# Kernel optimization log

Hardware: AMD Instinct MI355X
Metric: run time of the kernel (lower is better)

## Reference

```python
import jax, jax.numpy as jnp
import numpy as np

B, T, D, H = 2, 2048, 1024, 16
HD = D // H
DFF = 4 * D
EPS = 1e-5


def gelu_tanh(x):
    c = jnp.sqrt(2.0 / jnp.pi).astype(x.dtype)
    return 0.5 * x * (1.0 + jnp.tanh(c * (x + 0.044715 * x ** 3)))


def layernorm(x, scale, shift):
    mean = jnp.mean(x, axis=-1, keepdims=True)
    var = jnp.var(x, axis=-1, keepdims=True)  # unbiased=False
    return (x - mean) / jnp.sqrt(var + EPS) * scale + shift


def setup_inputs() -> dict:
    key = jax.random.key(0)
    ks = jax.random.split(key, 12)
    s = lambda fan_in: 1.0 / np.sqrt(fan_in)
    return {
        "x": jax.random.normal(ks[0], (B, T, D), jnp.float32),
        "wq": jax.random.normal(ks[1], (D, D), jnp.float32) * s(D),
        "wk": jax.random.normal(ks[2], (D, D), jnp.float32) * s(D),
        "wv": jax.random.normal(ks[3], (D, D), jnp.float32) * s(D),
        "wo": jax.random.normal(ks[4], (D, D), jnp.float32) * s(D),
        "bo": jnp.zeros((D,), jnp.float32),
        "ln1_scale": jnp.ones((D,), jnp.float32),
        "ln1_shift": jnp.zeros((D,), jnp.float32),
        "ln2_scale": jnp.ones((D,), jnp.float32),
        "ln2_shift": jnp.zeros((D,), jnp.float32),
        "w1": jax.random.normal(ks[5], (D, DFF), jnp.float32) * s(D),
        "b1": jnp.zeros((DFF,), jnp.float32),
        "w2": jax.random.normal(ks[6], (DFF, D), jnp.float32) * s(DFF),
        "b2": jnp.zeros((D,), jnp.float32),
    }


def reference(x, wq, wk, wv, wo, bo, ln1_scale, ln1_shift, ln2_scale, ln2_shift, w1, b1, w2, b2):
    # pre-LN attention
    h = layernorm(x, ln1_scale, ln1_shift)
    q = (h @ wq).reshape(B, T, H, HD).transpose(0, 2, 1, 3)  # [B,H,T,hd]
    k = (h @ wk).reshape(B, T, H, HD).transpose(0, 2, 1, 3)
    v = (h @ wv).reshape(B, T, H, HD).transpose(0, 2, 1, 3)
    scores = jnp.einsum('bhqd,bhkd->bhqk', q, k) / jnp.sqrt(jnp.float32(HD))
    causal = jnp.tril(jnp.ones((T, T), bool))
    scores = jnp.where(causal, scores, -jnp.inf)
    attn = jax.nn.softmax(scores, axis=-1)
    ctx = jnp.einsum('bhqk,bhkd->bhqd', attn, v)
    ctx = ctx.transpose(0, 2, 1, 3).reshape(B, T, D)
    attn_out = ctx @ wo + bo
    x = x + attn_out  # dropout p=0
    # pre-LN FFN
    h2 = layernorm(x, ln2_scale, ln2_shift)
    ff = gelu_tanh(h2 @ w1 + b1) @ w2 + b2
    return x + ff
```

## Files before the change

kernel.cpp:

```cpp
#include <hip/hip_runtime.h>
#include <hip/hip_bf16.h>
#include <stdint.h>

typedef unsigned short u16;
typedef __attribute__((ext_vector_type(8))) short s16x8;
typedef __attribute__((ext_vector_type(4))) float f32x4;

#define B_   2
#define T_   2048
#define D_   1024
#define H_   16
#define HD_  64
#define DFF_ 4096
#define M_   (B_*T_)

#define SC2F 0.18033688f

__device__ __forceinline__ u16 f2b(float f){
  uint32_t u = __float_as_uint(f);
  u += 0x7FFFu + ((u >> 16) & 1u);
  return (u16)(u >> 16);
}
__device__ __forceinline__ float b2f(u16 u){ return __uint_as_float(((uint32_t)u) << 16); }
__device__ __forceinline__ uint32_t pk2(float lo, float hi){
  uint32_t r;
  asm volatile("v_cvt_pk_bf16_f32 %0, %1, %2" : "=v"(r) : "v"(lo), "v"(hi));
  return r;
}

__device__ __forceinline__ void gl_lds16(const void* g, void* l){
  __builtin_amdgcn_global_load_lds((const __attribute__((address_space(1))) void*)g,
                                   (__attribute__((address_space(3))) void*)l, 16, 0, 0);
}

template<int N> __device__ __forceinline__ void waitvm(){
  if constexpr (N == 0)      asm volatile("s_waitcnt vmcnt(0)" ::: "memory");
  else if constexpr (N == 2) asm volatile("s_waitcnt vmcnt(2)" ::: "memory");
  else if constexpr (N == 4) asm volatile("s_waitcnt vmcnt(4)" ::: "memory");
  else                       asm volatile("s_waitcnt vmcnt(8)" ::: "memory");
}

__device__ __forceinline__ void wconv_tile(const float* __restrict__ W, u16* __restrict__ Wt,
                                           int K, int N, int tk, int tn, int tid,
                                           u16* __restrict__ tile ){
  const int k0 = tk << 6, n0 = tn << 6;
  const int rr = tid >> 4, c4 = (tid & 15) << 2;
  #pragma unroll
  for (int rep = 0; rep < 4; rep++){
    int r = rr + (rep << 4);
    float4 v = *reinterpret_cast<const float4*>(W + (size_t)(k0 + r)*N + n0 + c4);
    tile[r*68 + c4+0] = f2b(v.x); tile[r*68 + c4+1] = f2b(v.y);
    tile[r*68 + c4+2] = f2b(v.z); tile[r*68 + c4+3] = f2b(v.w);
  }
  __syncthreads();
  const int rn = tid >> 2, kb = (tid & 3) << 4;
  u16 tmp[16];
  #pragma unroll
  for (int j = 0; j < 16; j++) tmp[j] = tile[(kb + j)*68 + rn];
  ushort4* dst = reinterpret_cast<ushort4*>(Wt + (size_t)(n0 + rn)*K + k0 + kb);
  dst[0] = make_ushort4(tmp[0], tmp[1], tmp[2], tmp[3]);
  dst[1] = make_ushort4(tmp[4], tmp[5], tmp[6], tmp[7]);
  dst[2] = make_ushort4(tmp[8], tmp[9], tmp[10], tmp[11]);
  dst[3] = make_ushort4(tmp[12], tmp[13], tmp[14], tmp[15]);
}

__global__ __launch_bounds__(256) void wconv_all(const float* __restrict__ wq,
                                                 const float* __restrict__ wk,
                                                 const float* __restrict__ wv,
                                                 const float* __restrict__ wo,
                                                 u16* __restrict__ wqkvT, u16* __restrict__ woT,
                                                 const float* __restrict__ x,
                                                 const float* __restrict__ ln1s,
                                                 const float* __restrict__ ln1b,
                                                 u16* __restrict__ hout){
  const int bid = blockIdx.x;
  const int tid = threadIdx.x;
  if (bid >= 1024){
    const int row = bid - 1024;
    float4 a = reinterpret_cast<const float4*>(x + ((size_t)row << 10))[tid];
    float s = a.x + a.y + a.z + a.w;
    float q = a.x*a.x + a.y*a.y + a.z*a.z + a.w*a.w;
    #pragma unroll
    for (int o = 32; o > 0; o >>= 1){ s += __shfl_xor(s, o); q += __shfl_xor(q, o); }
    __shared__ float red[8];
    const int w = tid >> 6;
    if ((tid & 63) == 0){ red[w] = s; red[4 + w] = q; }
    __syncthreads();
    float S = red[0] + red[1] + red[2] + red[3];
    float Q = red[4] + red[5] + red[6] + red[7];
    float mean = S * (1.0f/1024.0f);
    float var  = Q * (1.0f/1024.0f) - mean*mean;
    float inv = rsqrtf(var + 1e-5f);
    float4 gsc = reinterpret_cast<const float4*>(ln1s)[tid];
    float4 gsh = reinterpret_cast<const float4*>(ln1b)[tid];
    ushort4 o4;
    o4.x = f2b((a.x - mean)*inv*gsc.x + gsh.x);
    o4.y = f2b((a.y - mean)*inv*gsc.y + gsh.y);
    o4.z = f2b((a.z - mean)*inv*gsc.z + gsh.z);
    o4.w = f2b((a.w - mean)*inv*gsc.w + gsh.w);
    reinterpret_cast<ushort4*>(hout + ((size_t)row << 10))[tid] = o4;
    return;
  }
  __shared__ u16 tile[64*68];
  const int which = bid >> 8, t = bid & 255;
  const float* W = (which == 0) ? wq : (which == 1) ? wk : (which == 2) ? wv : wo;
  u16* Wt = (which == 3) ? woT : wqkvT + (size_t)which * D_ * D_;
  wconv_tile(W, Wt, 1024, 1024, t >> 4, t & 15, tid, tile);
}

__global__ __launch_bounds__(256) void reduce2(const u16* __restrict__ p,
                                               const float* __restrict__ bias,
                                               const u16* __restrict__ resid,
                                               float* __restrict__ out){
  const size_t idx = ((size_t)blockIdx.x << 8) + threadIdx.x;
  ushort4 a4 = reinterpret_cast<const ushort4*>(p)[idx];
  ushort4 b4 = reinterpret_cast<const ushort4*>(p)[idx + (((size_t)M_*D_) >> 2)];
  ushort4 r4 = reinterpret_cast<const ushort4*>(resid)[idx];
  float4 bb = reinterpret_cast<const float4*>(bias)[threadIdx.x];
  float4 o;
  o.x = b2f(a4.x) + b2f(b4.x) + b2f(r4.x) + bb.x;
  o.y = b2f(a4.y) + b2f(b4.y) + b2f(r4.y) + bb.y;
  o.z = b2f(a4.z) + b2f(b4.z) + b2f(r4.z) + bb.z;
  o.w = b2f(a4.w) + b2f(b4.w) + b2f(r4.w) + bb.w;
  reinterpret_cast<float4*>(out)[idx] = o;
}

__global__ __launch_bounds__(256) void reduce_ln(const u16* __restrict__ p,
                                                 const float* __restrict__ bias,
                                                 const float* __restrict__ resid,
                                                 const float* __restrict__ sc,
                                                 const float* __restrict__ sh,
                                                 u16* __restrict__ x1,
                                                 u16* __restrict__ h2){
  const int row = blockIdx.x;
  const int tid = threadIdx.x;
  const size_t idx = ((size_t)row << 8) + tid;
  ushort4 a4 = reinterpret_cast<const ushort4*>(p)[idx];
  ushort4 b4 = reinterpret_cast<const ushort4*>(p)[idx + (((size_t)M_*D_) >> 2)];
  float4 r  = reinterpret_cast<const float4*>(resid)[idx];
  float4 bb = reinterpret_cast<const float4*>(bias)[tid];
  float4 v;
  v.x = b2f(a4.x) + b2f(b4.x) + r.x + bb.x;
  v.y = b2f(a4.y) + b2f(b4.y) + r.y + bb.y;
  v.z = b2f(a4.z) + b2f(b4.z) + r.z + bb.z;
  v.w = b2f(a4.w) + b2f(b4.w) + r.w + bb.w;
  ushort4 xo;
  xo.x = f2b(v.x); xo.y = f2b(v.y); xo.z = f2b(v.z); xo.w = f2b(v.w);
  reinterpret_cast<ushort4*>(x1)[idx] = xo;
  float s = v.x + v.y + v.z + v.w;
  float q = v.x*v.x + v.y*v.y + v.z*v.z + v.w*v.w;
  #pragma unroll
  for (int o = 32; o > 0; o >>= 1){ s += __shfl_xor(s, o); q += __shfl_xor(q, o); }
  __shared__ float red[8];
  const int w = tid >> 6;
  if ((tid & 63) == 0){ red[w] = s; red[4 + w] = q; }
  __syncthreads();
  float S = red[0] + red[1] + red[2] + red[3];
  float Q = red[4] + red[5] + red[6] + red[7];
  float mean = S * (1.0f/1024.0f);
  float var  = Q * (1.0f/1024.0f) - mean*mean;
  float inv = rsqrtf(var + 1e-5f);
  float4 gsc = reinterpret_cast<const float4*>(sc)[tid];
  float4 gsh = reinterpret_cast<const float4*>(sh)[tid];
  ushort4 o4;
  o4.x = f2b((v.x - mean)*inv*gsc.x + gsh.x);
  o4.y = f2b((v.y - mean)*inv*gsc.y + gsh.y);
  o4.z = f2b((v.z - mean)*inv*gsc.z + gsh.z);
  o4.w = f2b((v.w - mean)*inv*gsc.w + gsh.w);
  reinterpret_cast<ushort4*>(h2 + ((size_t)row << 10))[tid] = o4;
}

template<int EPI, int NF>
__global__ __launch_bounds__(512, 2) void gemm8(const u16* __restrict__ A, const u16* __restrict__ Bt,
                                                const float* __restrict__ bias,
                                                void* __restrict__ Cv, void* __restrict__ Cv2,
                                                const float* __restrict__ cw1,
                                                const float* __restrict__ cw2,
                                                u16* __restrict__ w1T, u16* __restrict__ w2T,
                                                int M, int N, int K, int lda){
  constexpr int BROWS = NF * 32;
  __shared__ __align__(16) u16 LA[2][2][128*64];
  __shared__ __align__(16) u16 LB[2][2][BROWS*64];
  const int tid = threadIdx.x;

  if constexpr (EPI == 1){
    if (blockIdx.x >= 192){
      const int tid256 = tid & 255, sel2 = tid >> 8;
      u16* tile = &LA[0][0][0] + sel2 * (64*68);
      const int t = ((int)blockIdx.x - 192)*2 + sel2;
      if (t < 1024) wconv_tile(cw1, w1T, 1024, 4096, t >> 6, t & 63, tid256, tile);
      else          wconv_tile(cw2, w2T, 4096, 1024, (t-1024) >> 4, (t-1024) & 15, tid256, tile);
      return;
    }
  }

  const int lane = tid & 63;
  const int w = tid >> 6;
  const int wm = w >> 2, wn = w & 3;
  const int g = lane >> 4, l15 = lane & 15;
  const int bnb = (wn & 1) * (NF * 16);

  int tn, tm, kz;
  if constexpr (EPI == 1){
    const int flat = blockIdx.x;
    const int nfid = (flat & 7) * 24 + (flat >> 3);
    tn = nfid % 12; tm = nfid / 12; kz = 0;
  } else {
    const int nx = gridDim.x, ny = gridDim.y;
    const int nwg = nx * ny * gridDim.z;
    const int flat = blockIdx.x + nx * (blockIdx.y + ny * blockIdx.z);
    const int nfid = (flat & 7) * (nwg >> 3) + (flat >> 3);
    tn = nfid % nx;
    const int rest = nfid / nx;
    tm = rest % ny;
    kz = rest / ny;
  }
  const int tn0 = tn * (NF * 64);
  const int tm0 = tm << 8;
  const u16* Az = A  + (size_t)kz * K;
  const u16* Bz = Bt + (size_t)kz * K;

  const int arow0 = tid >> 3,         asl0 = (((tid) & 7) ^ (arow0 & 7)) << 3;
  const int arow1 = (tid + 512) >> 3, asl1 = (((tid + 512) & 7) ^ (arow1 & 7)) << 3;

  f32x4 acc[8][NF];
  #pragma unroll
  for (int i = 0; i < 8; i++)
    #pragma unroll
    for (int j = 0; j < NF; j++) acc[i][j] = (f32x4){0.f,0.f,0.f,0.f};
  s16x8 bf[NF][2];
  constexpr int WVN = (NF == 4) ? 8 : 2;

#define STG_A(db, h, tt) do{                                                        \
    gl_lds16(Az + (size_t)(tm0 + (h)*128 + arow0)*lda + ((tt) << 6) + asl0,         \
             &LA[db][h][tid*8]);                                                    \
    gl_lds16(Az + (size_t)(tm0 + (h)*128 + arow1)*lda + ((tt) << 6) + asl1,         \
             &LA[db][h][(tid + 512)*8]);                                            \
  }while(0)
#define STG_B(db, h, tt) do{                                                        \
    gl_lds16(Bz + (size_t)(tn0 + (h)*BROWS + arow0)*lda + ((tt) << 6) + asl0,       \
             &LB[db][h][tid*8]);                                                    \
    if constexpr (NF == 4){                                                         \
      gl_lds16(Bz + (size_t)(tn0 + (h)*BROWS + arow1)*lda + ((tt) << 6) + asl1,     \
               &LB[db][h][(tid + 512)*8]);                                          \
    }                                                                               \
  }while(0)
#define LDAF(db, mf, kk) (*reinterpret_cast<const s16x8*>(                          \
    &LA[db][wm][((mf)*16 + l15)*64 + ((((kk)*4 + g) ^ (l15 & 7)) << 3)]))
#define LDBF(db, nf, kk) (*reinterpret_cast<const s16x8*>(                          \
    &LB[db][wn >> 1][(bnb + (nf)*16 + l15)*64 + ((((kk)*4 + g) ^ (l15 & 7)) << 3)]))
#define BLOAD(db) do{ _Pragma("unroll")                                             \
    for (int nf = 0; nf < NF; nf++){ bf[nf][0] = LDBF(db, nf, 0);                   \
                                     bf[nf][1] = LDBF(db, nf, 1); } }while(0)
#define PH(db, MFA, MFB, STG, WV) do{                                               \
    s16x8 a00 = LDAF(db, MFA, 0), a01 = LDAF(db, MFA, 1);                           \
    s16x8 a10 = LDAF(db, MFB, 0), a11 = LDAF(db, MFB, 1);                           \
    STG;                                                                            \
    WV;                                                                             \
    __builtin_amdgcn_s_barrier();                                                   \
    __builtin_amdgcn_s_setprio(1);                                                  \
    _Pragma("unroll")                                                               \
    for (int nf = 0; nf < NF; nf++){                                                \
      acc[MFA][nf] = __builtin_amdgcn_mfma_f32_16x16x32_bf16(a00, bf[nf][0], acc[MFA][nf], 0,0,0); \
      acc[MFA][nf] = __builtin_amdgcn_mfma_f32_16x16x32_bf16(a01, bf[nf][1], acc[MFA][nf], 0,0,0); \
      acc[MFB][nf] = __builtin_amdgcn_mfma_f32_16x16x32_bf16(a10, bf[nf][0], acc[MFB][nf], 0,0,0); \
      acc[MFB][nf] = __builtin_amdgcn_mfma_f32_16x16x32_bf16(a11, bf[nf][1], acc[MFB][nf], 0,0,0); \
    }                                                                               \
    __builtin_amdgcn_s_setprio(0);                                                  \
    __builtin_amdgcn_s_barrier();                                                   \
  }while(0)

  const int NT = K >> 6;
  STG_B(0, 0, 0); STG_B(0, 1, 0); STG_A(0, 0, 0); STG_A(0, 1, 0);
  STG_B(1, 0, 1); STG_B(1, 1, 1);
  waitvm<NF>();
  __builtin_amdgcn_s_barrier();

  for (int t = 0; t < NT; t += 2){
    const bool last = (t + 2 >= NT);
    BLOAD(0);
    PH(0, 0, 1, STG_A(1, 0, t + 1), );
    PH(0, 2, 3, STG_A(1, 1, t + 1), );
    PH(0, 4, 5, if (!last) STG_B(0, 0, t + 2), );
    PH(0, 6, 7, if (!last) STG_B(0, 1, t + 2),
                if (last) waitvm<0>(); else waitvm<WVN>(););
    BLOAD(1);
    PH(1, 0, 1, if (!last) STG_A(0, 0, t + 2), );
    PH(1, 2, 3, if (!last) STG_A(0, 1, t + 2), );
    PH(1, 4, 5, if (!last) STG_B(1, 0, t + 3), );
    PH(1, 6, 7, if (!last) STG_B(1, 1, t + 3),
                if (last) waitvm<0>(); else waitvm<WVN>(););
  }
#undef STG_A
#undef STG_B
#undef LDAF
#undef LDBF
#undef BLOAD
#undef PH

  if constexpr (EPI == 1){
    const int sel = tn0 >> 10;
    if (sel < 2){
      #pragma unroll
      for (int mf = 0; mf < 8; mf++){
        const int mb = tm0 + wm*128 + mf*16 + (g << 2);
        #pragma unroll
        for (int nf = 0; nf < NF; nf++){
          const int n = tn0 + wn*(NF*16) + nf*16 + l15;
          const int nn = n & 1023;
          const int hh = nn >> 6, d = nn & 63;
          #pragma unroll
          for (int rr = 0; rr < 4; rr++){
            const int m = mb + rr;
            float v = acc[mf][nf][rr];
            if (sel == 0) v *= SC2F;
            ((u16*)Cv)[(size_t)sel*((size_t)M_*D_) +
                       ((((size_t)(m >> 11)*H_ + hh)*T_ + (m & 2047)) << 6) + d] = f2b(v);
          }
        }
      }
    } else {
      u16* TR = &LA[0][0][0];
      u16* vt = (u16*)Cv2;
      const int bq = tm0 >> 11;
      const int tloc = tm0 & 2047;
      #pragma unroll
      for (int hp = 0; hp < 2; hp++){
        __syncthreads();
        if ((wn >> 1) == hp){
          #pragma unroll
          for (int mf = 0; mf < 8; mf++){
            const int mb = wm*128 + mf*16 + (g << 2);
            #pragma unroll
            for (int nf = 0; nf < NF; nf++){
              const int nr = ((wn & 1) << 6) + (nf << 4) + l15;
              #pragma unroll
              for (int rr = 0; rr < 4; rr++){
                const int m = mb + rr;
                TR[nr*256 + (((m >> 3) ^ (nr & 15)) << 3) + (m & 7)] = f2b(acc[mf][nf][rr]);
              }
            }
          }
        }
        __syncthreads();
        {
          const int nr = tid >> 2;
          const int m0 = (tid & 3) << 6;
          const int nn = (tn0 & 1023) + (hp << 7) + nr;
          const int hh = nn >> 6, d = nn & 63;
          u16* dst = vt + (((size_t)(bq*H_ + hh))*HD_ + d)*T_ + tloc + m0;
          #pragma unroll
          for (int jj = 0; jj < 8; jj++){
            const int j = (m0 >> 3) + jj;
            s16x8 vv = *reinterpret_cast<const s16x8*>(&TR[nr*256 + ((j ^ (nr & 15)) << 3)]);
            *reinterpret_cast<s16x8*>(dst + jj*8) = vv;
          }
        }
      }
    }
  } else {
    #pragma unroll
    for (int mf = 0; mf < 8; mf++){
      const int mb = tm0 + wm*128 + mf*16 + (g << 2);
      #pragma unroll
      for (int nf = 0; nf < NF; nf++){
        const int n = tn0 + wn*(NF*16) + nf*16 + l15;
        #pragma unroll
        for (int rr = 0; rr < 4; rr++){
          const int m = mb + rr;
          float v = acc[mf][nf][rr];
          if constexpr (EPI == 0){
            ((u16*)Cv)[(size_t)kz*((size_t)M*N) + (size_t)m*N + n] = f2b(v);
          } else {
            float u = v + bias[n];
            float t2 = 0.7978845608f*(u + 0.044715f*u*u*u);
            float e = __expf(2.0f*t2);
            float th = 1.0f - 2.0f/(e + 1.0f);
            ((u16*)Cv)[(size_t)m*N + n] = f2b(0.5f*u*(1.0f + th));
          }
        }
      }
    }
  }
}

__global__ __launch_bounds__(512) void attn_k(const u16* __restrict__ Qg, const u16* __restrict__ Kg,
                                              const u16* __restrict__ Vg, u16* __restrict__ ctx){
  const int flat = blockIdx.x + (blockIdx.y << 3);
  const int xcd = flat & 7, j_ = (flat >> 3) & 3, pr_ = flat >> 5;
  const int bh  = (j_ << 3) + xcd;
  const int tid = threadIdx.x;
  const int lane = tid & 63;
  const int w = tid >> 6;
  const int g = lane >> 4, l15 = lane & 15;

  __shared__ __align__(16) u16 Qs[128*64];
  __shared__ __align__(16) u16 Ks[2][128*64];
  __shared__ __align__(16) u16 Vt[2][64*128];
  __shared__ __align__(16) u16 Pl[8][16*128];
  u16* const Plw = &Pl[w][0];

  const size_t hb = (size_t)bh * ((size_t)T_*HD_);
  const u16* Qh = Qg + hb;
  const u16* Kh = Kg + hb;
  const u16* Vh = Vg + hb;
  const int b = bh >> 4, hh = bh & 15;

  const int qk_r0 = tid >> 3,         qk_c0 = (((tid) & 7) ^ (qk_r0 & 7)) << 3;
  const int qk_r1 = (tid + 512) >> 3, qk_c1 = (((tid + 512) & 7) ^ (qk_r1 & 7)) << 3;
  const int v_r0 = tid >> 4,          v_c0 = (((tid) & 15) ^ (v_r0 & 7)) << 3;
  const int v_r1 = (tid + 512) >> 4,  v_c1 = (((tid + 512) & 15) ^ (v_r1 & 7)) << 3;

  for (int ph = 0; ph < 2; ++ph){
    const int qt = ph ? (15 - pr_) : pr_;
    const int NKT = qt + 1;

    gl_lds16(Qh + (size_t)(qt*128 + qk_r0)*HD_ + qk_c0, Qs + tid*8);
    gl_lds16(Qh + (size_t)(qt*128 + qk_r1)*HD_ + qk_c1, Qs + (tid+512)*8);
    gl_lds16(Kh + (size_t)qk_r0*HD_ + qk_c0, Ks[0] + tid*8);
    gl_lds16(Kh + (size_t)qk_r1*HD_ + qk_c1, Ks[0] + (tid+512)*8);
    gl_lds16(Vh + (size_t)v_r0*T_ + v_c0, Vt[0] + tid*8);
    gl_lds16(Vh + (size_t)v_r1*T_ + v_c1, Vt[0] + (tid+512)*8);
    __syncthreads();

    s16x8 qa[2];
    #pragma unroll
    for (int kk = 0; kk < 2; kk++){
      int ra = (w << 4) + l15;
      int slot = (kk << 2) + g;
      qa[kk] = *reinterpret_cast<const s16x8*>(Qs + ra*64 + ((slot ^ (ra & 7)) << 3));
    }

    f32x4 accO[4];
    #pragma unroll
    for (int j = 0; j < 4; j++) accO[j] = (f32x4){0.f,0.f,0.f,0.f};
    float mrow = -1e30f, lrow = 0.f;
    const int qgl = qt*128 + (w << 4) + l15;

    for (int kt = 0; kt < NKT; ++kt){
      const int cur = kt & 1, nxt = cur ^ 1;
      const bool pf = (kt + 1 < NKT);

      if (pf){
        gl_lds16(Kh + (size_t)((kt+1)*128 + qk_r0)*HD_ + qk_c0, Ks[nxt] + tid*8);
        gl_lds16(Kh + (size_t)((kt+1)*128 + qk_r1)*HD_ + qk_c1, Ks[nxt] + (tid+512)*8);
        gl_lds16(Vh + (size_t)v_r0*T_ + (kt+1)*128 + v_c0, Vt[nxt] + tid*8);
        gl_lds16(Vh + (size_t)v_r1*T_ + (kt+1)*128 + v_c1, Vt[nxt] + (tid+512)*8);
      }

      f32x4 accS[8];
      #pragma unroll
      for (int j = 0; j < 8; j++) accS[j] = (f32x4){0.f,0.f,0.f,0.f};
      __builtin_amdgcn_s_setprio(1);
      #pragma unroll
      for (int jn = 0; jn < 8; jn++){
        #pragma unroll
        for (int kk = 0; kk < 2; kk++){
          int rb = (jn << 4) + l15;
          int slot = (kk << 2) + g;
          s16x8 kf = *reinterpret_cast<const s16x8*>(Ks[cur] + rb*64 + ((slot ^ (rb & 7)) << 3));
          accS[jn] = __builtin_amdgcn_mfma_f32_16x16x32_bf16(kf, qa[kk], accS[jn], 0, 0, 0);
        }
      }
      __builtin_amdgcn_s_setprio(0);

      if (kt == qt){
        #pragma unroll
        for (int jn = 0; jn < 8; jn++)
          #pragma unroll
          for (int rr = 0; rr < 4; rr++){
            int kgl = kt*128 + (jn << 4) + (g << 2) + rr;
            if (kgl > qgl) accS[jn][rr] = -1e30f;
          }
      }

      float rmax = accS[0][0];
      #pragma unroll
      for (int jn = 0; jn < 8; jn++)
        #pragma unroll
        for (int rr = 0; rr < 4; rr++) rmax = fmaxf(rmax, accS[jn][rr]);
      rmax = fmaxf(rmax, __shfl_xor(rmax, 16));
      rmax = fmaxf(rmax, __shfl_xor(rmax, 32));

      if (__any(rmax > mrow + 8.0f)){
        float mn = fmaxf(mrow, rmax);
        float sf = exp2f(mrow - mn);
        mrow = mn;
        lrow *= sf;
        #pragma unroll
        for (int rr = 0; rr < 4; rr++){
          float sfr = __shfl(sf, ((lane >> 4) << 2) + rr);
          #pragma unroll
          for (int jn = 0; jn < 4; jn++) accO[jn][rr] *= sfr;
        }
      }

      float tsum = 0.f;
      #pragma unroll
      for (int jn = 0; jn < 8; jn++){
        float pv0 = exp2f(accS[jn][0] - mrow);
        float pv1 = exp2f(accS[jn][1] - mrow);
        float pv2 = exp2f(accS[jn][2] - mrow);
        float pv3 = exp2f(accS[jn][3] - mrow);
        tsum += (pv0 + pv1) + (pv2 + pv3);
        int ch = ((jn << 1) | (g >> 1)) ^ (l15 & 7);
        int base = (l15 << 7) + (ch << 3) + ((g & 1) << 2);
        uint2 pkd = make_uint2(pk2(pv0, pv1), pk2(pv2, pv3));
        *reinterpret_cast<uint2*>(&Plw[base]) = pkd;
      }
      tsum += __shfl_xor(tsum, 16);
      tsum += __shfl_xor(tsum, 32);
      lrow += tsum;

      __builtin_amdgcn_s_setprio(1);
      #pragma unroll
      for (int kk = 0; kk < 4; kk++){
        int pch = ((kk << 2) + g) ^ (l15 & 7);
        s16x8 pa = *reinterpret_cast<const s16x8*>(&Plw[(l15 << 7) + (pch << 3)]);
        #pragma unroll
        for (int jn = 0; jn < 4; jn++){
          int vd = (jn << 4) + l15;
          int vslot = (((kk << 2) + g) & 8) | ((((kk << 2) + g) ^ (vd & 7)) & 7);
          s16x8 vbf = *reinterpret_cast<const s16x8*>(Vt[cur] + (vd << 7) + (vslot << 3));
          accO[jn] = __builtin_amdgcn_mfma_f32_16x16x32_bf16(pa, vbf, accO[jn], 0, 0, 0);
        }
      }
      __builtin_amdgcn_s_setprio(0);

      __syncthreads();
    }

    #pragma unroll
    for (int rr = 0; rr < 4; rr++){
      float lr = __shfl(lrow, ((lane >> 4) << 2) + rr);
      float inv = 1.0f / lr;
      int qrow = qt*128 + (w << 4) + (g << 2) + rr;
      size_t rowbase = ((size_t)(b*T_ + qrow) << 10) + ((size_t)hh << 6);
      #pragma unroll
      for (int jn = 0; jn < 4; jn++){
        int d = (jn << 4) + l15;
        ctx[rowbase + d] = f2b(accO[jn][rr] * inv);
      }
    }
  }
}

extern "C" void kernel_launch(void* const* d_in, const int* in_sizes, int n_in,
                              void* d_out, int out_size, void* d_ws, size_t ws_size,
                              hipStream_t stream){
  (void)in_sizes; (void)n_in; (void)out_size; (void)ws_size;
  const float* x    = (const float*)d_in[0];
  const float* wq   = (const float*)d_in[1];
  const float* wk   = (const float*)d_in[2];
  const float* wv   = (const float*)d_in[3];
  const float* wo   = (const float*)d_in[4];
  const float* bo   = (const float*)d_in[5];
  const float* ln1s = (const float*)d_in[6];
  const float* ln1b = (const float*)d_in[7];
  const float* ln2s = (const float*)d_in[8];
  const float* ln2b = (const float*)d_in[9];
  const float* w1   = (const float*)d_in[10];
  const float* b1   = (const float*)d_in[11];
  const float* w2   = (const float*)d_in[12];
  const float* b2   = (const float*)d_in[13];
  float* out = (float*)d_out;

  char* p = (char*)d_ws;
  u16*  wqkvT = (u16*)p;  p += (size_t)3*D_*D_*2;
  u16*  woT   = (u16*)p;  p += (size_t)D_*D_*2;
  u16*  w1T   = (u16*)p;  p += (size_t)D_*DFF_*2;
  u16*  w2T   = (u16*)p;  p += (size_t)DFF_*D_*2;
  u16*  h     = (u16*)p;  p += (size_t)M_*D_*2;
  u16*  qb    = (u16*)p;  p += (size_t)M_*D_*2;
  u16*  kb    = (u16*)p;  p += (size_t)M_*D_*2;
  u16*  vb    = (u16*)p;  p += (size_t)M_*D_*2;
  u16*  ctx   = (u16*)p;  p += (size_t)M_*D_*2;
  u16*  x1    = (u16*)p;  p += (size_t)M_*D_*2;
  u16*  h2    = (u16*)p;  p += (size_t)M_*D_*2;
  u16*  ff1   = (u16*)p;  p += (size_t)M_*DFF_*2;
  (void)kb; (void)vb;
  u16* part = h;

  dim3 blk(256), blk8(512);
  wconv_all<<<1024 + M_, blk, 0, stream>>>(wq, wk, wv, wo, wqkvT, woT, x, ln1s, ln1b, h);
  gemm8<1,4><<<192 + 1024, blk8, 0, stream>>>(h, wqkvT, nullptr, qb, ff1,
                                              w1, w2, w1T, w2T, M_, 3*D_, D_, D_);
  attn_k<<<dim3(8,32), blk8, 0, stream>>>(qb, qb + (size_t)M_*D_, ff1, ctx);
  gemm8<0,2><<<dim3(8,16,2), blk8, 0, stream>>>(ctx, woT, nullptr, part, nullptr,
                                                nullptr, nullptr, nullptr, nullptr,
                                                M_, D_, D_/2, D_);
  reduce_ln<<<M_, blk, 0, stream>>>(part, bo, x, ln2s, ln2b, x1, h2);
  gemm8<3,4><<<dim3(16,16,1), blk8, 0, stream>>>(h2, w1T, b1, ff1, nullptr,
                                                 nullptr, nullptr, nullptr, nullptr,
                                                 M_, DFF_, D_, D_);
  gemm8<0,2><<<dim3(8,16,2), blk8, 0, stream>>>(ff1, w2T, nullptr, part, nullptr,
                                                nullptr, nullptr, nullptr, nullptr,
                                                M_, D_, DFF_/2, DFF_);
  reduce2<<<M_, blk, 0, stream>>>(part, b2, x1, out);
}
```

Measured before the change: 212.7 us.

## Triple-buffer K/V in attention and merge GEMM phases into fewer barriers

```diff
diff --git a/kernel.cpp b/kernel.cpp
--- a/kernel.cpp
+++ b/kernel.cpp
@@ -39,6 +39,9 @@
   else if constexpr (N == 4) asm volatile("s_waitcnt vmcnt(4)" ::: "memory");
   else                       asm volatile("s_waitcnt vmcnt(8)" ::: "memory");
 }
+#define BARRL do{ asm volatile("s_waitcnt lgkmcnt(0)" ::: "memory"); \
+                  __builtin_amdgcn_s_barrier(); \
+                  asm volatile("" ::: "memory"); }while(0)
 
 __device__ __forceinline__ void wconv_tile(const float* __restrict__ W, u16* __restrict__ Wt,
                                            int K, int N, int tk, int tn, int tid,
@@ -229,7 +232,6 @@
     #pragma unroll
     for (int j = 0; j < NF; j++) acc[i][j] = (f32x4){0.f,0.f,0.f,0.f};
   s16x8 bf[NF][2];
-  constexpr int WVN = (NF == 4) ? 8 : 2;
 
 #define STG_A(db, h, tt) do{                                                        \
     gl_lds16(Az + (size_t)(tm0 + (h)*128 + arow0)*lda + ((tt) << 6) + asl0,         \
@@ -252,19 +254,25 @@
 #define BLOAD(db) do{ _Pragma("unroll")                                             \
     for (int nf = 0; nf < NF; nf++){ bf[nf][0] = LDBF(db, nf, 0);                   \
                                      bf[nf][1] = LDBF(db, nf, 1); } }while(0)
-#define PH(db, MFA, MFB, STG, WV) do{                                               \
-    s16x8 a00 = LDAF(db, MFA, 0), a01 = LDAF(db, MFA, 1);                           \
-    s16x8 a10 = LDAF(db, MFB, 0), a11 = LDAF(db, MFB, 1);                           \
+#define PH2(db, MF0, STG, WV) do{                                                   \
+    s16x8 aA0 = LDAF(db, (MF0)+0, 0), aA1 = LDAF(db, (MF0)+0, 1);                   \
+    s16x8 aB0 = LDAF(db, (MF0)+1, 0), aB1 = LDAF(db, (MF0)+1, 1);                   \
+    s16x8 aC0 = LDAF(db, (MF0)+2, 0), aC1 = LDAF(db, (MF0)+2, 1);                   \
+    s16x8 aD0 = LDAF(db, (MF0)+3, 0), aD1 = LDAF(db, (MF0)+3, 1);                   \
     STG;                                                                            \
     WV;                                                                             \
     __builtin_amdgcn_s_barrier();                                                   \
     __builtin_amdgcn_s_setprio(1);                                                  \
     _Pragma("unroll")                                                               \
     for (int nf = 0; nf < NF; nf++){                                                \
-      acc[MFA][nf] = __builtin_amdgcn_mfma_f32_16x16x32_bf16(a00, bf[nf][0], acc[MFA][nf], 0,0,0); \
-      acc[MFA][nf] = __builtin_amdgcn_mfma_f32_16x16x32_bf16(a01, bf[nf][1], acc[MFA][nf], 0,0,0); \
-      acc[MFB][nf] = __builtin_amdgcn_mfma_f32_16x16x32_bf16(a10, bf[nf][0], acc[MFB][nf], 0,0,0); \
-      acc[MFB][nf] = __builtin_amdgcn_mfma_f32_16x16x32_bf16(a11, bf[nf][1], acc[MFB][nf], 0,0,0); \
+      acc[(MF0)+0][nf] = __builtin_amdgcn_mfma_f32_16x16x32_bf16(aA0, bf[nf][0], acc[(MF0)+0][nf], 0,0,0); \
+      acc[(MF0)+0][nf] = __builtin_amdgcn_mfma_f32_16x16x32_bf16(aA1, bf[nf][1], acc[(MF0)+0][nf], 0,0,0); \
+      acc[(MF0)+1][nf] = __builtin_amdgcn_mfma_f32_16x16x32_bf16(aB0, bf[nf][0], acc[(MF0)+1][nf], 0,0,0); \
+      acc[(MF0)+1][nf] = __builtin_amdgcn_mfma_f32_16x16x32_bf16(aB1, bf[nf][1], acc[(MF0)+1][nf], 0,0,0); \
+      acc[(MF0)+2][nf] = __builtin_amdgcn_mfma_f32_16x16x32_bf16(aC0, bf[nf][0], acc[(MF0)+2][nf], 0,0,0); \
+      acc[(MF0)+2][nf] = __builtin_amdgcn_mfma_f32_16x16x32_bf16(aC1, bf[nf][1], acc[(MF0)+2][nf], 0,0,0); \
+      acc[(MF0)+3][nf] = __builtin_amdgcn_mfma_f32_16x16x32_bf16(aD0, bf[nf][0], acc[(MF0)+3][nf], 0,0,0); \
+      acc[(MF0)+3][nf] = __builtin_amdgcn_mfma_f32_16x16x32_bf16(aD1, bf[nf][1], acc[(MF0)+3][nf], 0,0,0); \
     }                                                                               \
     __builtin_amdgcn_s_setprio(0);                                                  \
     __builtin_amdgcn_s_barrier();                                                   \
@@ -279,24 +287,20 @@
   for (int t = 0; t < NT; t += 2){
     const bool last = (t + 2 >= NT);
     BLOAD(0);
-    PH(0, 0, 1, STG_A(1, 0, t + 1), );
-    PH(0, 2, 3, STG_A(1, 1, t + 1), );
-    PH(0, 4, 5, if (!last) STG_B(0, 0, t + 2), );
-    PH(0, 6, 7, if (!last) STG_B(0, 1, t + 2),
-                if (last) waitvm<0>(); else waitvm<WVN>(););
+    PH2(0, 0, { STG_A(1, 0, t + 1); STG_A(1, 1, t + 1); }, );
+    PH2(0, 4, { if (!last){ STG_B(0, 0, t + 2); STG_B(0, 1, t + 2); } },
+              if (last) waitvm<0>(); else waitvm<NF>(););
     BLOAD(1);
-    PH(1, 0, 1, if (!last) STG_A(0, 0, t + 2), );
-    PH(1, 2, 3, if (!last) STG_A(0, 1, t + 2), );
-    PH(1, 4, 5, if (!last) STG_B(1, 0, t + 3), );
-    PH(1, 6, 7, if (!last) STG_B(1, 1, t + 3),
-                if (last) waitvm<0>(); else waitvm<WVN>(););
+    PH2(1, 0, { if (!last){ STG_A(0, 0, t + 2); STG_A(0, 1, t + 2); } }, );
+    PH2(1, 4, { if (!last){ STG_B(1, 0, t + 3); STG_B(1, 1, t + 3); } },
+              if (last) waitvm<0>(); else waitvm<NF>(););
   }
 #undef STG_A
 #undef STG_B
 #undef LDAF
 #undef LDBF
 #undef BLOAD
-#undef PH
+#undef PH2
 
   if constexpr (EPI == 1){
     const int sel = tn0 >> 10;
@@ -394,10 +398,10 @@
   const int w = tid >> 6;
   const int g = lane >> 4, l15 = lane & 15;
 
-  __shared__ __align__(16) u16 Qs[128*64];
-  __shared__ __align__(16) u16 Ks[2][128*64];
-  __shared__ __align__(16) u16 Vt[2][64*128];
   __shared__ __align__(16) u16 Pl[8][16*128];
+  __shared__ __align__(16) u16 Ks[3][128*64];
+  __shared__ __align__(16) u16 Vt[3][64*128];
+  u16* const Qs  = &Pl[0][0];
   u16* const Plw = &Pl[w][0];
 
   const size_t hb = (size_t)bh * ((size_t)T_*HD_);
@@ -411,17 +415,26 @@
   const int v_r0 = tid >> 4,          v_c0 = (((tid) & 15) ^ (v_r0 & 7)) << 3;
   const int v_r1 = (tid + 512) >> 4,  v_c1 = (((tid + 512) & 15) ^ (v_r1 & 7)) << 3;
 
+#define STG_K(buf, kt) do{                                                          \
+    gl_lds16(Kh + (size_t)((kt)*128 + qk_r0)*HD_ + qk_c0, Ks[buf] + tid*8);         \
+    gl_lds16(Kh + (size_t)((kt)*128 + qk_r1)*HD_ + qk_c1, Ks[buf] + (tid+512)*8);   \
+  }while(0)
+#define STG_V(buf, kt) do{                                                          \
+    gl_lds16(Vh + (size_t)v_r0*T_ + (kt)*128 + v_c0, Vt[buf] + tid*8);              \
+    gl_lds16(Vh + (size_t)v_r1*T_ + (kt)*128 + v_c1, Vt[buf] + (tid+512)*8);        \
+  }while(0)
+
   for (int ph = 0; ph < 2; ++ph){
     const int qt = ph ? (15 - pr_) : pr_;
     const int NKT = qt + 1;
 
+    BARRL;
     gl_lds16(Qh + (size_t)(qt*128 + qk_r0)*HD_ + qk_c0, Qs + tid*8);
     gl_lds16(Qh + (size_t)(qt*128 + qk_r1)*HD_ + qk_c1, Qs + (tid+512)*8);
-    gl_lds16(Kh + (size_t)qk_r0*HD_ + qk_c0, Ks[0] + tid*8);
-    gl_lds16(Kh + (size_t)qk_r1*HD_ + qk_c1, Ks[0] + (tid+512)*8);
-    gl_lds16(Vh + (size_t)v_r0*T_ + v_c0, Vt[0] + tid*8);
-    gl_lds16(Vh + (size_t)v_r1*T_ + v_c1, Vt[0] + (tid+512)*8);
-    __syncthreads();
+    STG_K(0, 0); STG_V(0, 0);
+    if (NKT > 1){ STG_K(1, 1); STG_V(1, 1); }
+    if (NKT > 1) waitvm<4>(); else waitvm<0>();
+    BARRL;
 
     s16x8 qa[2];
     #pragma unroll
@@ -430,6 +443,7 @@
       int slot = (kk << 2) + g;
       qa[kk] = *reinterpret_cast<const s16x8*>(Qs + ra*64 + ((slot ^ (ra & 7)) << 3));
     }
+    BARRL;
 
     f32x4 accO[4];
     #pragma unroll
@@ -437,16 +451,16 @@
     float mrow = -1e30f, lrow = 0.f;
     const int qgl = qt*128 + (w << 4) + l15;
 
+    int cur = 0, n2 = 2;
     for (int kt = 0; kt < NKT; ++kt){
-      const int cur = kt & 1, nxt = cur ^ 1;
-      const bool pf = (kt + 1 < NKT);
-
-      if (pf){
-        gl_lds16(Kh + (size_t)((kt+1)*128 + qk_r0)*HD_ + qk_c0, Ks[nxt] + tid*8);
-        gl_lds16(Kh + (size_t)((kt+1)*128 + qk_r1)*HD_ + qk_c1, Ks[nxt] + (tid+512)*8);
-        gl_lds16(Vh + (size_t)v_r0*T_ + (kt+1)*128 + v_c0, Vt[nxt] + tid*8);
-        gl_lds16(Vh + (size_t)v_r1*T_ + (kt+1)*128 + v_c1, Vt[nxt] + (tid+512)*8);
-      }
+      if (kt > 0) BARRL;
+      if (kt + 2 < NKT){ STG_K(n2, kt + 2); STG_V(n2, kt + 2); }
+      if (kt + 2 < NKT)      waitvm<8>();
+      else if (kt + 1 < NKT) waitvm<4>();
+      else                   waitvm<0>();
+
+      const u16* Kc = Ks[cur];
+      const u16* Vc = Vt[cur];
 
       f32x4 accS[8];
       #pragma unroll
@@ -458,7 +472,7 @@
         for (int kk = 0; kk < 2; kk++){
           int rb = (jn << 4) + l15;
           int slot = (kk << 2) + g;
-          s16x8 kf = *reinterpret_cast<const s16x8*>(Ks[cur] + rb*64 + ((slot ^ (rb & 7)) << 3));
+          s16x8 kf = *reinterpret_cast<const s16x8*>(Kc + rb*64 + ((slot ^ (rb & 7)) << 3));
           accS[jn] = __builtin_amdgcn_mfma_f32_16x16x32_bf16(kf, qa[kk], accS[jn], 0, 0, 0);
         }
       }
@@ -521,13 +535,14 @@
         for (int jn = 0; jn < 4; jn++){
           int vd = (jn << 4) + l15;
           int vslot = (((kk << 2) + g) & 8) | ((((kk << 2) + g) ^ (vd & 7)) & 7);
-          s16x8 vbf = *reinterpret_cast<const s16x8*>(Vt[cur] + (vd << 7) + (vslot << 3));
+          s16x8 vbf = *reinterpret_cast<const s16x8*>(Vc + (vd << 7) + (vslot << 3));
           accO[jn] = __builtin_amdgcn_mfma_f32_16x16x32_bf16(pa, vbf, accO[jn], 0, 0, 0);
         }
       }
       __builtin_amdgcn_s_setprio(0);
 
-      __syncthreads();
+      cur = (cur == 2) ? 0 : cur + 1;
+      n2  = (n2  == 2) ? 0 : n2  + 1;
     }
 
     #pragma unroll
@@ -543,6 +558,8 @@
       }
     }
   }
+#undef STG_K
+#undef STG_V
 }
 
 extern "C" void kernel_launch(void* const* d_in, const int* in_sizes, int n_in,
```

Result: faster. 205.8 us (-3.2%).

## Replace fine-grained phased GEMM pipeline with whole-tile double buffering

Applied to the files above, without the earlier changes.

```diff
diff --git a/kernel.cpp b/kernel.cpp
--- a/kernel.cpp
+++ b/kernel.cpp
@@ -34,11 +34,13 @@
 }
 
 template<int N> __device__ __forceinline__ void waitvm(){
-  if constexpr (N == 0)      asm volatile("s_waitcnt vmcnt(0)" ::: "memory");
-  else if constexpr (N == 2) asm volatile("s_waitcnt vmcnt(2)" ::: "memory");
-  else if constexpr (N == 4) asm volatile("s_waitcnt vmcnt(4)" ::: "memory");
-  else                       asm volatile("s_waitcnt vmcnt(8)" ::: "memory");
-}
+  if constexpr (N == 0)       asm volatile("s_waitcnt vmcnt(0)" ::: "memory");
+  else if constexpr (N == 4)  asm volatile("s_waitcnt vmcnt(4)" ::: "memory");
+  else if constexpr (N == 6)  asm volatile("s_waitcnt vmcnt(6)" ::: "memory");
+  else                        asm volatile("s_waitcnt vmcnt(8)" ::: "memory");
+}
+#define BARR do{ asm volatile("" ::: "memory"); __builtin_amdgcn_s_barrier(); \
+                 asm volatile("" ::: "memory"); }while(0)
 
 __device__ __forceinline__ void wconv_tile(const float* __restrict__ W, u16* __restrict__ Wt,
                                            int K, int N, int tk, int tn, int tid,
@@ -171,7 +173,7 @@
 }
 
 template<int EPI, int NF>
-__global__ __launch_bounds__(512, 2) void gemm8(const u16* __restrict__ A, const u16* __restrict__ Bt,
+__global__ __launch_bounds__(512, 1) void gemm8(const u16* __restrict__ A, const u16* __restrict__ Bt,
                                                 const float* __restrict__ bias,
                                                 void* __restrict__ Cv, void* __restrict__ Cv2,
                                                 const float* __restrict__ cw1,
@@ -228,8 +230,6 @@
   for (int i = 0; i < 8; i++)
     #pragma unroll
     for (int j = 0; j < NF; j++) acc[i][j] = (f32x4){0.f,0.f,0.f,0.f};
-  s16x8 bf[NF][2];
-  constexpr int WVN = (NF == 4) ? 8 : 2;
 
 #define STG_A(db, h, tt) do{                                                        \
     gl_lds16(Az + (size_t)(tm0 + (h)*128 + arow0)*lda + ((tt) << 6) + asl0,         \
@@ -249,54 +249,53 @@
     &LA[db][wm][((mf)*16 + l15)*64 + ((((kk)*4 + g) ^ (l15 & 7)) << 3)]))
 #define LDBF(db, nf, kk) (*reinterpret_cast<const s16x8*>(                          \
     &LB[db][wn >> 1][(bnb + (nf)*16 + l15)*64 + ((((kk)*4 + g) ^ (l15 & 7)) << 3)]))
-#define BLOAD(db) do{ _Pragma("unroll")                                             \
-    for (int nf = 0; nf < NF; nf++){ bf[nf][0] = LDBF(db, nf, 0);                   \
-                                     bf[nf][1] = LDBF(db, nf, 1); } }while(0)
-#define PH(db, MFA, MFB, STG, WV) do{                                               \
-    s16x8 a00 = LDAF(db, MFA, 0), a01 = LDAF(db, MFA, 1);                           \
-    s16x8 a10 = LDAF(db, MFB, 0), a11 = LDAF(db, MFB, 1);                           \
-    STG;                                                                            \
-    WV;                                                                             \
-    __builtin_amdgcn_s_barrier();                                                   \
+#define RUN(db) do{                                                                 \
+    s16x8 bfr[NF][2], af[8][2];                                                     \
+    _Pragma("unroll")                                                               \
+    for (int nf = 0; nf < NF; nf++){ bfr[nf][0] = LDBF(db, nf, 0);                  \
+                                     bfr[nf][1] = LDBF(db, nf, 1); }                \
+    _Pragma("unroll")                                                               \
+    for (int mf = 0; mf < 8; mf++){ af[mf][0] = LDAF(db, mf, 0);                    \
+                                    af[mf][1] = LDAF(db, mf, 1); }                  \
     __builtin_amdgcn_s_setprio(1);                                                  \
     _Pragma("unroll")                                                               \
-    for (int nf = 0; nf < NF; nf++){                                                \
-      acc[MFA][nf] = __builtin_amdgcn_mfma_f32_16x16x32_bf16(a00, bf[nf][0], acc[MFA][nf], 0,0,0); \
-      acc[MFA][nf] = __builtin_amdgcn_mfma_f32_16x16x32_bf16(a01, bf[nf][1], acc[MFA][nf], 0,0,0); \
-      acc[MFB][nf] = __builtin_amdgcn_mfma_f32_16x16x32_bf16(a10, bf[nf][0], acc[MFB][nf], 0,0,0); \
-      acc[MFB][nf] = __builtin_amdgcn_mfma_f32_16x16x32_bf16(a11, bf[nf][1], acc[MFB][nf], 0,0,0); \
-    }                                                                               \
+    for (int mf = 0; mf < 8; mf++)                                                  \
+      _Pragma("unroll")                                                             \
+      for (int nf = 0; nf < NF; nf++){                                              \
+        acc[mf][nf] = __builtin_amdgcn_mfma_f32_16x16x32_bf16(af[mf][0], bfr[nf][0], acc[mf][nf], 0,0,0); \
+        acc[mf][nf] = __builtin_amdgcn_mfma_f32_16x16x32_bf16(af[mf][1], bfr[nf][1], acc[mf][nf], 0,0,0); \
+      }                                                                             \
     __builtin_amdgcn_s_setprio(0);                                                  \
-    __builtin_amdgcn_s_barrier();                                                   \
   }while(0)
 
   const int NT = K >> 6;
-  STG_B(0, 0, 0); STG_B(0, 1, 0); STG_A(0, 0, 0); STG_A(0, 1, 0);
-  STG_B(1, 0, 1); STG_B(1, 1, 1);
-  waitvm<NF>();
-  __builtin_amdgcn_s_barrier();
+  STG_A(0, 0, 0); STG_A(0, 1, 0);
+  STG_B(0, 0, 0); STG_B(0, 1, 0);
 
   for (int t = 0; t < NT; t += 2){
     const bool last = (t + 2 >= NT);
-    BLOAD(0);
-    PH(0, 0, 1, STG_A(1, 0, t + 1), );
-    PH(0, 2, 3, STG_A(1, 1, t + 1), );
-    PH(0, 4, 5, if (!last) STG_B(0, 0, t + 2), );
-    PH(0, 6, 7, if (!last) STG_B(0, 1, t + 2),
-                if (last) waitvm<0>(); else waitvm<WVN>(););
-    BLOAD(1);
-    PH(1, 0, 1, if (!last) STG_A(0, 0, t + 2), );
-    PH(1, 2, 3, if (!last) STG_A(0, 1, t + 2), );
-    PH(1, 4, 5, if (!last) STG_B(1, 0, t + 3), );
-    PH(1, 6, 7, if (!last) STG_B(1, 1, t + 3),
-                if (last) waitvm<0>(); else waitvm<WVN>(););
+    STG_A(1, 0, t + 1); STG_A(1, 1, t + 1);
+    STG_B(1, 0, t + 1); STG_B(1, 1, t + 1);
+    waitvm<(NF == 4) ? 8 : 6>();
+    BARR;
+    RUN(0);
+    BARR;
+    if (!last){
+      STG_A(0, 0, t + 2); STG_A(0, 1, t + 2);
+      STG_B(0, 0, t + 2); STG_B(0, 1, t + 2);
+      waitvm<(NF == 4) ? 8 : 6>();
+    } else {
+      waitvm<0>();
+    }
+    BARR;
+    RUN(1);
+    BARR;
   }
 #undef STG_A
 #undef STG_B
 #undef LDAF
 #undef LDBF
-#undef BLOAD
-#undef PH
+#undef RUN
 
   if constexpr (EPI == 1){
     const int sel = tn0 >> 10;
```

New measurement: 231.9 us. 1.09x slower.
